# Kernel optimization log

Measured on AMD Instinct MI355X. Metric: run time of the kernel, lower is better.

The kernel has to match this reference:

```python
import jax, jax.numpy as jnp
import numpy as np

B, C, K, H, W = 8, 64, 32, 128, 128  # K = num_cluster // 2
NEG_SLOPE = 0.1


def setup_inputs() -> dict:
    key = jax.random.key(0)
    k1, k2, k3, k4, k5, k6 = jax.random.split(key, 6)
    HR = jax.random.normal(k1, (B, C, H, W), jnp.float32)
    LR = jax.random.normal(k2, (B, C, H, W), jnp.float32)
    # Conv2d(1+K, 1, 1) weights flattened to [1+K] + bias, Conv2d(1,1,1) -> scalar w/b
    w1 = jax.random.normal(k3, (K + 1,), jnp.float32) * 0.1
    b1 = jax.random.normal(k4, (1,), jnp.float32) * 0.1
    w2 = jax.random.normal(k5, (1,), jnp.float32) * 0.1
    b2 = jax.random.normal(k6, (1,), jnp.float32) * 0.1
    return {"HR": HR, "LR": LR, "w1": w1, "b1": b1, "w2": w2, "b2": b2}


def reference(HR, LR, w1, b1, w2, b2):
    Bn, Cn = HR.shape[0], HR.shape[1]
    HRf = HR.reshape(Bn, Cn, -1)                      # [B, C, HW]
    LRf = LR.reshape(Bn, Cn, -1)                      # [B, C, HW]
    corr = jnp.einsum('bcn,bdn->bcd', LRf, HRf)       # [B, C_lr, C_hr]
    _, idx = jax.lax.top_k(corr, K)                   # [B, C, K] (int32)
    # gather top-K HR channels per LR channel: [B, C, K, H, W]
    gathered = jax.vmap(lambda h, ix: h[ix])(HR, idx)
    weight = jax.nn.sigmoid(jnp.max(gathered, axis=2))        # [B, C, H, W]
    # 1x1 conv over the (1+K) concatenated channels == weighted sum
    fusion = w1[0] * LR + jnp.einsum('bckhw,k->bchw', gathered, w1[1:]) + b1[0]
    fusion = jnp.where(fusion >= 0, fusion, NEG_SLOPE * fusion)  # LeakyReLU(0.1)
    fusion = w2[0] * fusion + b2[0]                   # second 1x1 conv
    return fusion * (1.0 + weight)                    # fusion + weight*fusion
```

## Files before the change

kernel.cpp:

```cpp
#include <hip/hip_runtime.h>
#include <math.h>

#define B_ 8
#define C_ 64
#define K_ 32
#define HW_ 16384
#define LDN 132
#define NCHUNKOUT_ 64
#define TILE_ 256
#define NEG_SLOPE_ 0.1f


__global__ __launch_bounds__(256, 2) void corr_partial_kernel(
    const float* __restrict__ LR, const float* __restrict__ HR,
    float* __restrict__ partial)
{
    __shared__ float smem[16896];
    float* lrS = smem;
    float* hrS = smem + C_ * LDN;

    const int bid = blockIdx.x;
    const int b = bid >> 6;
    const int q = bid & 63;
    const int t = threadIdx.x;
    const int wv = t >> 6;
    const int lane = t & 63;
    const int cq = lane >> 3;
    const int dq = lane & 7;

    float acc[8][8] = {};

    for (int r = 0; r < 2; ++r) {
        const int n0 = q * 256 + r * 128;
        if (r) __syncthreads();
        #pragma unroll
        for (int p = 0; p < 8; ++p) {
            const int f = p * 256 + t;
            const int c = f >> 5;
            const int col = (f & 31) * 4;
            *reinterpret_cast<float4*>(&lrS[c * LDN + col]) =
                *reinterpret_cast<const float4*>(&LR[(size_t)(b * C_ + c) * HW_ + n0 + col]);
            *reinterpret_cast<float4*>(&hrS[c * LDN + col]) =
                *reinterpret_cast<const float4*>(&HR[(size_t)(b * C_ + c) * HW_ + n0 + col]);
        }
        __syncthreads();

        #pragma unroll 2
        for (int nq = 0; nq < 8; ++nq) {
            const int col = wv * 32 + nq * 4;
            float4 lv[8];
            #pragma unroll
            for (int i = 0; i < 8; ++i)
                lv[i] = *reinterpret_cast<const float4*>(&lrS[(cq + 8 * i) * LDN + col]);
            #pragma unroll
            for (int j = 0; j < 8; ++j) {
                const float4 hv = *reinterpret_cast<const float4*>(&hrS[(dq + 8 * j) * LDN + col]);
                #pragma unroll
                for (int i = 0; i < 8; ++i) {
                    acc[i][j] = fmaf(lv[i].x, hv.x, acc[i][j]);
                    acc[i][j] = fmaf(lv[i].y, hv.y, acc[i][j]);
                    acc[i][j] = fmaf(lv[i].z, hv.z, acc[i][j]);
                    acc[i][j] = fmaf(lv[i].w, hv.w, acc[i][j]);
                }
            }
        }
    }

    __syncthreads();
    float* red = smem;
    #pragma unroll
    for (int i = 0; i < 8; ++i)
        #pragma unroll
        for (int j = 0; j < 8; ++j)
            red[(wv * 64 + i * 8 + j) * 64 + lane] = acc[i][j];
    __syncthreads();

    float* P = partial + (size_t)bid * (C_ * C_);
    #pragma unroll
    for (int pp = 0; pp < 16; ++pp) {
        const int p = wv * 16 + pp;
        const float s = ((red[(0 * 64 + p) * 64 + lane]
                        + red[(1 * 64 + p) * 64 + lane])
                        + red[(2 * 64 + p) * 64 + lane])
                        + red[(3 * 64 + p) * 64 + lane];
        const int row = cq + 8 * (p >> 3);
        const int col = dq + 8 * (p & 7);
        P[row * C_ + col] = s;
    }
}

__global__ __launch_bounds__(64) void rank_kernel(
    const float* __restrict__ partial, int* __restrict__ idxb)
{
    __shared__ double vals[C_];
    const int blk = blockIdx.x;
    const int b = blk >> 6;
    const int c = blk & 63;
    const int d = threadIdx.x;

    double acc = 0.0;
    for (int k = 0; k < NCHUNKOUT_; ++k)
        acc += (double)partial[(size_t)(b * NCHUNKOUT_ + k) * (C_ * C_) + c * C_ + d];
    vals[d] = acc;
    __syncthreads();

    int r = 0;
    for (int jj = 0; jj < C_; ++jj) {
        const double vj = vals[jj];
        r += (int)((vj > acc) || (vj == acc && jj < d));
    }
    if (r < K_) idxb[blk * K_ + r] = d;
}

__global__ __launch_bounds__(512, 4) void fusion_gather_kernel(
    const float* __restrict__ HR, const float* __restrict__ LR,
    const int* __restrict__ idxb,
    const float* __restrict__ w1, const float* __restrict__ b1,
    const float* __restrict__ w2, const float* __restrict__ b2,
    float* __restrict__ out)
{
    __shared__ float hrS[C_][TILE_];

    const int t = threadIdx.x;
    const int bid = blockIdx.x;
    const int b = bid >> 6;
    const int px0 = (bid & 63) * TILE_;

    const float* HRb = HR + (size_t)b * C_ * HW_;
    #pragma unroll
    for (int i = 0; i < 8; ++i) {
        const int f = i * 512 + t;
        const int c = f >> 6;
        const int qq = f & 63;
        *reinterpret_cast<float4*>(&hrS[c][qq * 4]) =
            *reinterpret_cast<const float4*>(&HRb[(size_t)c * HW_ + px0 + qq * 4]);
    }
    __syncthreads();

    const int wv = t >> 6;
    const int lane = t & 63;
    const int p4 = lane * 4;

    const int* idxc = idxb + b * C_ * K_;
    const float w10 = w1[0];
    const float b1v = b1[0], w2v = w2[0], b2v = b2[0];

    #pragma unroll 1
    for (int ci = 0; ci < 8; ++ci) {
        const int c = wv * 8 + ci;
        const float4 l4 = *reinterpret_cast<const float4*>(
            &LR[(size_t)(b * C_ + c) * HW_ + px0 + p4]);
        float acc[4] = {0.f, 0.f, 0.f, 0.f};
        float mx[4]  = {-1e30f, -1e30f, -1e30f, -1e30f};
        #pragma unroll
        for (int k = 0; k < K_; ++k) {
            const int d = idxc[c * K_ + k];
            const float4 h = *reinterpret_cast<const float4*>(&hrS[d][p4]);
            const float wk = w1[k + 1];
            acc[0] = fmaf(h.x, wk, acc[0]);
            acc[1] = fmaf(h.y, wk, acc[1]);
            acc[2] = fmaf(h.z, wk, acc[2]);
            acc[3] = fmaf(h.w, wk, acc[3]);
            mx[0] = fmaxf(mx[0], h.x);
            mx[1] = fmaxf(mx[1], h.y);
            mx[2] = fmaxf(mx[2], h.z);
            mx[3] = fmaxf(mx[3], h.w);
        }
        const float l[4] = {l4.x, l4.y, l4.z, l4.w};
        float o[4];
        #pragma unroll
        for (int p = 0; p < 4; ++p) {
            float f = fmaf(w10, l[p], acc[p]) + b1v;
            f = f >= 0.f ? f : NEG_SLOPE_ * f;
            f = fmaf(w2v, f, b2v);
            const float s = 1.f / (1.f + __expf(-mx[p]));
            o[p] = f * (1.f + s);
        }
        *reinterpret_cast<float4*>(&out[(size_t)(b * C_ + c) * HW_ + px0 + p4]) =
            make_float4(o[0], o[1], o[2], o[3]);
    }
}

extern "C" void kernel_launch(void* const* d_in, const int* in_sizes, int n_in,
                              void* d_out, int out_size, void* d_ws, size_t ws_size,
                              hipStream_t stream)
{
    const float* HR = (const float*)d_in[0];
    const float* LR = (const float*)d_in[1];
    const float* w1 = (const float*)d_in[2];
    const float* b1 = (const float*)d_in[3];
    const float* w2 = (const float*)d_in[4];
    const float* b2 = (const float*)d_in[5];
    float* out = (float*)d_out;

    float* partial = (float*)d_ws;
    int* idxb = (int*)((char*)d_ws + (size_t)B_ * NCHUNKOUT_ * C_ * C_ * sizeof(float));

    corr_partial_kernel<<<B_ * 64, 256, 0, stream>>>(LR, HR, partial);
    rank_kernel<<<B_ * C_, 64, 0, stream>>>(partial, idxb);
    fusion_gather_kernel<<<B_ * (HW_ / TILE_), 512, 0, stream>>>(HR, LR, idxb, w1, b1, w2, b2, out);
}
```

Baseline: 60.40 us.

## Use direct global-to-LDS loads with XOR swizzle and 512-thread correlation blocks

Reworks the correlation partial kernel so global tiles are copied straight into LDS with global_load_lds, using an XOR-swizzled layout in place of row padding to avoid bank conflicts. Block size doubles to 512 threads (8 waves), each wave covering a narrower column slice, and the cross-wave reduction is split into two phases of float4 writes so it fits the smaller shared buffer. The aim is to cut register staging and bank conflicts and raise occupancy. The cost is extra reduction traffic across 8 waves, and correctness depends on the swizzle matching the per-lane LDS destination layout.

```diff
diff --git a/kernel.cpp b/kernel.cpp
--- a/kernel.cpp
+++ b/kernel.cpp
@@ -5,19 +5,25 @@
 #define C_ 64
 #define K_ 32
 #define HW_ 16384
-#define LDN 132
 #define NCHUNKOUT_ 64
 #define TILE_ 256
 #define NEG_SLOPE_ 0.1f
 
 
-__global__ __launch_bounds__(256, 2) void corr_partial_kernel(
+__device__ __forceinline__ void gl_lds16(const float* g, float* l) {
+    __builtin_amdgcn_global_load_lds(
+        (const __attribute__((address_space(1))) void*)g,
+        (__attribute__((address_space(3))) void*)l,
+        16, 0, 0);
+}
+
+__global__ __launch_bounds__(512, 4) void corr_partial_kernel(
     const float* __restrict__ LR, const float* __restrict__ HR,
     float* __restrict__ partial)
 {
-    __shared__ float smem[16896];
+    __shared__ float smem[16384];
     float* lrS = smem;
-    float* hrS = smem + C_ * LDN;
+    float* hrS = smem + 8192;
 
     const int bid = blockIdx.x;
     const int b = bid >> 6;
@@ -30,31 +36,34 @@
 
     float acc[8][8] = {};
 
-    for (int r = 0; r < 2; ++r) {
-        const int n0 = q * 256 + r * 128;
-        if (r) __syncthreads();
-        #pragma unroll
-        for (int p = 0; p < 8; ++p) {
-            const int f = p * 256 + t;
-            const int c = f >> 5;
-            const int col = (f & 31) * 4;
-            *reinterpret_cast<float4*>(&lrS[c * LDN + col]) =
-                *reinterpret_cast<const float4*>(&LR[(size_t)(b * C_ + c) * HW_ + n0 + col]);
-            *reinterpret_cast<float4*>(&hrS[c * LDN + col]) =
-                *reinterpret_cast<const float4*>(&HR[(size_t)(b * C_ + c) * HW_ + n0 + col]);
+    #pragma unroll 1
+    for (int it = 0; it < 2; ++it) {
+        const int n0 = q * 256 + it * 128;
+        if (it) __syncthreads();
+
+        #pragma unroll
+        for (int s = 0; s < 4; ++s) {
+            const int r0 = wv * 8 + s * 2;
+            const int row = r0 + (lane >> 5);
+            const int cl = (((lane & 31) * 4) ^ ((row & 7) * 4));
+            const size_t goff = (size_t)(b * C_ + row) * HW_ + n0 + cl;
+            gl_lds16(&LR[goff], &lrS[r0 * 128]);
+            gl_lds16(&HR[goff], &hrS[r0 * 128]);
         }
         __syncthreads();
 
-        #pragma unroll 2
-        for (int nq = 0; nq < 8; ++nq) {
-            const int col = wv * 32 + nq * 4;
+        #pragma unroll
+        for (int nq = 0; nq < 4; ++nq) {
+            const int col = wv * 16 + nq * 4;
+            const int cxl = col ^ (cq * 4);
+            const int cxh = col ^ (dq * 4);
             float4 lv[8];
             #pragma unroll
             for (int i = 0; i < 8; ++i)
-                lv[i] = *reinterpret_cast<const float4*>(&lrS[(cq + 8 * i) * LDN + col]);
+                lv[i] = *reinterpret_cast<const float4*>(&lrS[(cq + 8 * i) * 128 + cxl]);
             #pragma unroll
             for (int j = 0; j < 8; ++j) {
-                const float4 hv = *reinterpret_cast<const float4*>(&hrS[(dq + 8 * j) * LDN + col]);
+                const float4 hv = *reinterpret_cast<const float4*>(&hrS[(dq + 8 * j) * 128 + cxh]);
                 #pragma unroll
                 for (int i = 0; i < 8; ++i) {
                     acc[i][j] = fmaf(lv[i].x, hv.x, acc[i][j]);
@@ -66,26 +75,37 @@
         }
     }
 
-    __syncthreads();
     float* red = smem;
-    #pragma unroll
-    for (int i = 0; i < 8; ++i)
-        #pragma unroll
-        for (int j = 0; j < 8; ++j)
-            red[(wv * 64 + i * 8 + j) * 64 + lane] = acc[i][j];
-    __syncthreads();
-
     float* P = partial + (size_t)bid * (C_ * C_);
-    #pragma unroll
-    for (int pp = 0; pp < 16; ++pp) {
-        const int p = wv * 16 + pp;
-        const float s = ((red[(0 * 64 + p) * 64 + lane]
-                        + red[(1 * 64 + p) * 64 + lane])
-                        + red[(2 * 64 + p) * 64 + lane])
-                        + red[(3 * 64 + p) * 64 + lane];
-        const int row = cq + 8 * (p >> 3);
-        const int col = dq + 8 * (p & 7);
-        P[row * C_ + col] = s;
+    #pragma unroll 1
+    for (int ph = 0; ph < 2; ++ph) {
+        __syncthreads();
+        #pragma unroll
+        for (int sl = 0; sl < 8; ++sl) {
+            const int i = ph * 4 + (sl >> 1);
+            const int j0 = (sl & 1) * 4;
+            *reinterpret_cast<float4*>(&red[((wv * 8 + sl) * 64 + lane) * 4]) =
+                make_float4(acc[i][j0], acc[i][j0 + 1], acc[i][j0 + 2], acc[i][j0 + 3]);
+        }
+        __syncthreads();
+        {
+            const int sl = t >> 6;
+            float4 s = make_float4(0.f, 0.f, 0.f, 0.f);
+            #pragma unroll
+            for (int w = 0; w < 8; ++w) {
+                const float4 v = *reinterpret_cast<const float4*>(
+                    &red[((w * 8 + sl) * 64 + lane) * 4]);
+                s.x += v.x; s.y += v.y; s.z += v.z; s.w += v.w;
+            }
+            const int i = ph * 4 + (sl >> 1);
+            const int j0 = (sl & 1) * 4;
+            const int row = (lane >> 3) + 8 * i;
+            const int colb = (lane & 7) + 8 * j0;
+            P[row * C_ + colb]      = s.x;
+            P[row * C_ + colb + 8]  = s.y;
+            P[row * C_ + colb + 16] = s.z;
+            P[row * C_ + colb + 24] = s.w;
+        }
     }
 }
 
@@ -196,7 +216,7 @@
     float* partial = (float*)d_ws;
     int* idxb = (int*)((char*)d_ws + (size_t)B_ * NCHUNKOUT_ * C_ * C_ * sizeof(float));
 
-    corr_partial_kernel<<<B_ * 64, 256, 0, stream>>>(LR, HR, partial);
+    corr_partial_kernel<<<B_ * 64, 512, 0, stream>>>(LR, HR, partial);
     rank_kernel<<<B_ * C_, 64, 0, stream>>>(partial, idxb);
     fusion_gather_kernel<<<B_ * (HW_ / TILE_), 512, 0, stream>>>(HR, LR, idxb, w1, b1, w2, b2, out);
 }
```

After: 187.4 us. 3.1x slower.
